# Kernel tuning notes

Hardware: AMD Instinct MI355X
Metric: run time of the kernel (lower is better)

Reference implementation:

```python
import jax, jax.numpy as jnp
import numpy as np

B, N, E, ENT, D, H, L = 64, 2048, 32768, 100000, 256, 256, 512


def setup_inputs() -> dict:
    key = jax.random.key(0)
    ks = jax.random.split(key, 12)
    return {
        "neighbors": jax.random.randint(ks[0], (B, N), 0, ENT),
        "adj_row": jax.random.randint(ks[1], (B, E), 0, N),
        "adj_col": jax.random.randint(ks[2], (B, E), 0, N),
        "adj_val": jax.random.uniform(ks[3], (B, E), dtype=jnp.float32),
        "emb_table": jax.random.normal(ks[4], (ENT, D), dtype=jnp.float32),
        "W1": jax.random.normal(ks[5], (D, H), dtype=jnp.float32) * (1.0 / np.sqrt(H)),
        "b1": jax.random.normal(ks[6], (H,), dtype=jnp.float32) * 0.01,
        "W2": jax.random.normal(ks[7], (H, H), dtype=jnp.float32) * (1.0 / np.sqrt(H)),
        "b2": jax.random.normal(ks[8], (H,), dtype=jnp.float32) * 0.01,
        "fc1_w": jax.random.normal(ks[9], (H, H), dtype=jnp.float32) * (1.0 / np.sqrt(H)),
        "fc1_b": jax.random.normal(ks[10], (H,), dtype=jnp.float32) * 0.01,
        "cur_len": L,
    }


def _gcn_layer(x, W, b, adj_row, adj_col, adj_val):
    # x: [B,N,din] -> support: [B,N,dout]
    support = jnp.einsum("bnd,dh->bnh", x, W)
    # sparse adj @ support: gather columns, scale by edge value, scatter-add to rows
    gathered = jnp.take_along_axis(support, adj_col[:, :, None], axis=1)  # [B,E,h]
    weighted = gathered * adj_val[:, :, None]
    agg = jax.vmap(lambda r, g: jax.ops.segment_sum(g, r, num_segments=N))(adj_row, weighted)
    return agg + b


def reference(neighbors, adj_row, adj_col, adj_val, emb_table, W1, b1, W2, b2, fc1_w, fc1_b, cur_len):
    x = emb_table[neighbors]                                   # [B,N,D] embedding gather
    x = _gcn_layer(x, W1, b1, adj_row, adj_col, adj_val)       # GCN layer 1
    x = _gcn_layer(x, W2, b2, adj_row, adj_col, adj_val)       # GCN layer 2
    seq = x[:, :cur_len, :]                                    # keep cur_node prefix, padded to common L
    pooled = jnp.mean(seq, axis=1, keepdims=True)              # self.seq == 'mean'
    return jax.nn.relu(jnp.einsum("blh,ho->blo", pooled, fc1_w) + fc1_b)  # [B,1,H]
```

## Files before the change

### kernel.cpp

```cpp
#include <hip/hip_runtime.h>

#define B 64
#define N 2048
#define E 32768
#define D 256
#define H 256
#define GCH 16
#define SEG 8
#define EPB (E / SEG)

__global__ __launch_bounds__(512) void edge_w_kernel(
    const int* __restrict__ adj_row, const int* __restrict__ adj_col,
    const float* __restrict__ adj_val, const int* __restrict__ cur_len,
    float* __restrict__ w_part, float* __restrict__ sw_part)
{
    __shared__ float wloc[N];
    __shared__ float sred[8];
    const int b = blockIdx.x, seg = blockIdx.y, tid = threadIdx.x;
    const int L = *cur_len;

    ((float4*)wloc)[tid] = make_float4(0.f, 0.f, 0.f, 0.f);
    __syncthreads();

    const int base = b * E + seg * EPB;
    float svp = 0.f;
    #pragma unroll
    for (int k = 0; k < EPB / 512; ++k) {
        const int e = base + tid + k * 512;
        const int r = adj_row[e];
        if (r < L) {
            const float v = adj_val[e];
            atomicAdd(&wloc[adj_col[e]], v);
            svp += v;
        }
    }
    __syncthreads();

    float4* dst = (float4*)(w_part + ((size_t)b * SEG + seg) * N);
    dst[tid] = ((const float4*)wloc)[tid];

    for (int off = 32; off; off >>= 1) svp += __shfl_down(svp, off, 64);
    if ((tid & 63) == 0) sred[tid >> 6] = svp;
    __syncthreads();
    if (tid == 0) {
        float s = 0.f;
        #pragma unroll
        for (int i = 0; i < 8; ++i) s += sred[i];
        sw_part[b * SEG + seg] = s;
    }
}

__global__ __launch_bounds__(512) void edge_z_kernel(
    const int* __restrict__ adj_row, const int* __restrict__ adj_col,
    const float* __restrict__ adj_val, const float* __restrict__ w_part,
    float* __restrict__ z_part)
{
    __shared__ float wfull[N];
    __shared__ float zloc[N];
    const int b = blockIdx.x, seg = blockIdx.y, tid = threadIdx.x;

    const float4* wp4 = (const float4*)(w_part + (size_t)b * SEG * N);
    float4 s = make_float4(0.f, 0.f, 0.f, 0.f);
    #pragma unroll
    for (int sg = 0; sg < SEG; ++sg) {
        const float4 v = wp4[sg * (N / 4) + tid];
        s.x += v.x; s.y += v.y; s.z += v.z; s.w += v.w;
    }
    ((float4*)wfull)[tid] = s;
    ((float4*)zloc)[tid]  = make_float4(0.f, 0.f, 0.f, 0.f);
    __syncthreads();

    const int base = b * E + seg * EPB;
    #pragma unroll
    for (int k = 0; k < EPB / 512; ++k) {
        const int e = base + tid + k * 512;
        const float wv = wfull[adj_row[e]];
        if (wv != 0.f) atomicAdd(&zloc[adj_col[e]], wv * adj_val[e]);
    }
    __syncthreads();

    float4* dst = (float4*)(z_part + ((size_t)b * SEG + seg) * N);
    dst[tid] = ((const float4*)zloc)[tid];
}

__global__ __launch_bounds__(256) void gather_kernel(
    const int* __restrict__ neighbors, const float* __restrict__ emb,
    const float* __restrict__ z_part, float* __restrict__ u_part)
{
    const int b = blockIdx.x, grp = blockIdx.y, tid = threadIdx.x;
    const int lane = tid & 63, rg = tid >> 6;
    const int n0 = grp * 128;

    __shared__ float zh[2][128];
    __shared__ int   ns[128];
    {
        const int j = tid & 127, half = tid >> 7;
        float s = 0.f;
        #pragma unroll
        for (int sg = 0; sg < SEG / 2; ++sg)
            s += z_part[((size_t)b * SEG + half * (SEG / 2) + sg) * N + n0 + j];
        zh[half][j] = s;
        if (half == 0) ns[j] = neighbors[(size_t)b * N + n0 + j];
    }
    __syncthreads();

    const float4* __restrict__ emb4 = (const float4*)emb;
    float4 a0 = make_float4(0.f,0.f,0.f,0.f), a1 = a0, a2 = a0, a3 = a0;

    #pragma unroll 8
    for (int i = 0; i < 32; ++i) {
        const int j = i * 4 + rg;
        const float zv = zh[0][j] + zh[1][j];
        const size_t idx = (size_t)ns[j];
        const float4 v = emb4[idx * (D / 4) + lane];
        if ((i & 3) == 0)      { a0.x += zv*v.x; a0.y += zv*v.y; a0.z += zv*v.z; a0.w += zv*v.w; }
        else if ((i & 3) == 1) { a1.x += zv*v.x; a1.y += zv*v.y; a1.z += zv*v.z; a1.w += zv*v.w; }
        else if ((i & 3) == 2) { a2.x += zv*v.x; a2.y += zv*v.y; a2.z += zv*v.z; a2.w += zv*v.w; }
        else                   { a3.x += zv*v.x; a3.y += zv*v.y; a3.z += zv*v.z; a3.w += zv*v.w; }
    }
    float4 acc = make_float4(a0.x+a1.x+a2.x+a3.x, a0.y+a1.y+a2.y+a3.y,
                             a0.z+a1.z+a2.z+a3.z, a0.w+a1.w+a2.w+a3.w);

    __shared__ float4 red[256];
    red[tid] = acc;
    __syncthreads();
    if (tid < 64) {
        float4 a = red[tid], bb = red[tid + 64], c = red[tid + 128], d = red[tid + 192];
        float4 s = make_float4(a.x + bb.x + c.x + d.x, a.y + bb.y + c.y + d.y,
                               a.z + bb.z + c.z + d.z, a.w + bb.w + c.w + d.w);
        ((float4*)u_part)[((size_t)b * GCH + grp) * (D / 4) + tid] = s;
    }
}

__global__ __launch_bounds__(1024) void head_kernel(
    const float* __restrict__ u_part, const float* __restrict__ sw_part,
    const float* __restrict__ W1, const float* __restrict__ b1,
    const float* __restrict__ W2, const float* __restrict__ b2,
    const float* __restrict__ fc1_w, const float* __restrict__ fc1_b,
    const int* __restrict__ cur_len, float* __restrict__ out)
{
    const int b = blockIdx.x;
    const int t = threadIdx.x & 255;
    const int s = threadIdx.x >> 8;
    __shared__ float red[4][256];
    __shared__ float su[D];
    __shared__ float sy[H];
    __shared__ float sp[H];

    float part = 0.f;
    #pragma unroll
    for (int c = 0; c < GCH / 4; ++c)
        part += u_part[((size_t)b * GCH + s * (GCH / 4) + c) * D + t];
    red[s][t] = part;
    __syncthreads();
    if (s == 0) su[t] = red[0][t] + red[1][t] + red[2][t] + red[3][t];
    __syncthreads();

    part = 0.f;
    #pragma unroll 8
    for (int k = 0; k < 64; ++k) {
        const int d = s * 64 + k;
        part += su[d] * W1[d * H + t];
    }
    red[s][t] = part;
    __syncthreads();
    if (s == 0) {
        float sw = 0.f;
        #pragma unroll
        for (int i = 0; i < SEG; ++i) sw += sw_part[b * SEG + i];
        sy[t] = red[0][t] + red[1][t] + red[2][t] + red[3][t] + sw * b1[t];
    }
    __syncthreads();

    const float invL = 1.f / (float)(*cur_len);
    part = 0.f;
    #pragma unroll 8
    for (int k = 0; k < 64; ++k) {
        const int d = s * 64 + k;
        part += sy[d] * W2[d * H + t];
    }
    red[s][t] = part;
    __syncthreads();
    if (s == 0)
        sp[t] = (red[0][t] + red[1][t] + red[2][t] + red[3][t]) * invL + b2[t];
    __syncthreads();

    part = 0.f;
    #pragma unroll 8
    for (int k = 0; k < 64; ++k) {
        const int d = s * 64 + k;
        part += sp[d] * fc1_w[d * H + t];
    }
    red[s][t] = part;
    __syncthreads();
    if (s == 0) {
        const float v = red[0][t] + red[1][t] + red[2][t] + red[3][t] + fc1_b[t];
        out[(size_t)b * H + t] = fmaxf(v, 0.f);
    }
}

extern "C" void kernel_launch(void* const* d_in, const int* in_sizes, int n_in,
                              void* d_out, int out_size, void* d_ws, size_t ws_size,
                              hipStream_t stream) {
    const int*   neighbors = (const int*)  d_in[0];
    const int*   adj_row   = (const int*)  d_in[1];
    const int*   adj_col   = (const int*)  d_in[2];
    const float* adj_val   = (const float*)d_in[3];
    const float* emb_table = (const float*)d_in[4];
    const float* W1        = (const float*)d_in[5];
    const float* b1        = (const float*)d_in[6];
    const float* W2        = (const float*)d_in[7];
    const float* b2        = (const float*)d_in[8];
    const float* fc1_w     = (const float*)d_in[9];
    const float* fc1_b     = (const float*)d_in[10];
    const int*   cur_len   = (const int*)  d_in[11];
    float*       out       = (float*)d_out;

    float* wp_ws = (float*)d_ws;
    float* zp_ws = wp_ws + (size_t)B * SEG * N;
    float* sw_ws = zp_ws + (size_t)B * SEG * N;
    float* u_ws  = sw_ws + (size_t)B * SEG;

    edge_w_kernel<<<dim3(B, SEG), 512, 0, stream>>>(adj_row, adj_col, adj_val,
                                                    cur_len, wp_ws, sw_ws);
    edge_z_kernel<<<dim3(B, SEG), 512, 0, stream>>>(adj_row, adj_col, adj_val,
                                                    wp_ws, zp_ws);
    gather_kernel<<<dim3(B, GCH), 256, 0, stream>>>(neighbors, emb_table, zp_ws, u_ws);
    head_kernel<<<B, 1024, 0, stream>>>(u_ws, sw_ws, W1, b1, W2, b2,
                                        fc1_w, fc1_b, cur_len, out);
}
```

Before: 225.5 us.

## Fuse head MLP into gather kernel via last-block atomic counter

Removes the separate head kernel launch. Each gather block bumps a per-batch atomic counter, and the last block of each batch reduces the partial sums and runs the three small matvecs with 256 threads. The counter is reset in edge_w_kernel. This saves one launch and its gap, but the tail matvecs now run on 256 threads per batch instead of 1024, which lengthens the serial tail.

Result: slower. 386.8 us (+71.6%).

```diff
diff --git a/kernel.cpp b/kernel.cpp
--- a/kernel.cpp
+++ b/kernel.cpp
@@ -12,13 +12,15 @@
 __global__ __launch_bounds__(512) void edge_w_kernel(
     const int* __restrict__ adj_row, const int* __restrict__ adj_col,
     const float* __restrict__ adj_val, const int* __restrict__ cur_len,
-    float* __restrict__ w_part, float* __restrict__ sw_part)
+    float* __restrict__ w_part, float* __restrict__ sw_part,
+    int* __restrict__ cnt)
 {
     __shared__ float wloc[N];
     __shared__ float sred[8];
     const int b = blockIdx.x, seg = blockIdx.y, tid = threadIdx.x;
     const int L = *cur_len;
 
+    if (seg == 0 && tid == 0) cnt[b] = 0;
     ((float4*)wloc)[tid] = make_float4(0.f, 0.f, 0.f, 0.f);
     __syncthreads();
 
@@ -83,9 +85,14 @@
     dst[tid] = ((const float4*)zloc)[tid];
 }
 
-__global__ __launch_bounds__(256) void gather_kernel(
+__global__ __launch_bounds__(256) void gather_head_kernel(
     const int* __restrict__ neighbors, const float* __restrict__ emb,
-    const float* __restrict__ z_part, float* __restrict__ u_part)
+    const float* __restrict__ z_part, float* __restrict__ u_part,
+    int* __restrict__ cnt, const float* __restrict__ sw_part,
+    const float* __restrict__ W1, const float* __restrict__ b1,
+    const float* __restrict__ W2, const float* __restrict__ b2,
+    const float* __restrict__ fc1_w, const float* __restrict__ fc1_b,
+    const int* __restrict__ cur_len, float* __restrict__ out)
 {
     const int b = blockIdx.x, grp = blockIdx.y, tid = threadIdx.x;
     const int lane = tid & 63, rg = tid >> 6;
@@ -130,73 +137,48 @@
                                a.z + bb.z + c.z + d.z, a.w + bb.w + c.w + d.w);
         ((float4*)u_part)[((size_t)b * GCH + grp) * (D / 4) + tid] = s;
     }
-}
-
-__global__ __launch_bounds__(1024) void head_kernel(
-    const float* __restrict__ u_part, const float* __restrict__ sw_part,
-    const float* __restrict__ W1, const float* __restrict__ b1,
-    const float* __restrict__ W2, const float* __restrict__ b2,
-    const float* __restrict__ fc1_w, const float* __restrict__ fc1_b,
-    const int* __restrict__ cur_len, float* __restrict__ out)
-{
-    const int b = blockIdx.x;
-    const int t = threadIdx.x & 255;
-    const int s = threadIdx.x >> 8;
-    __shared__ float red[4][256];
+    __syncthreads();
+
+    __shared__ int is_last;
+    __threadfence();
+    if (tid == 0) is_last = (atomicAdd(&cnt[b], 1) == GCH - 1) ? 1 : 0;
+    __syncthreads();
+    if (!is_last) return;
+    __threadfence();
+
     __shared__ float su[D];
     __shared__ float sy[H];
     __shared__ float sp[H];
-
-    float part = 0.f;
-    #pragma unroll
-    for (int c = 0; c < GCH / 4; ++c)
-        part += u_part[((size_t)b * GCH + s * (GCH / 4) + c) * D + t];
-    red[s][t] = part;
-    __syncthreads();
-    if (s == 0) su[t] = red[0][t] + red[1][t] + red[2][t] + red[3][t];
-    __syncthreads();
-
-    part = 0.f;
-    #pragma unroll 8
-    for (int k = 0; k < 64; ++k) {
-        const int d = s * 64 + k;
-        part += su[d] * W1[d * H + t];
-    }
-    red[s][t] = part;
-    __syncthreads();
-    if (s == 0) {
-        float sw = 0.f;
-        #pragma unroll
-        for (int i = 0; i < SEG; ++i) sw += sw_part[b * SEG + i];
-        sy[t] = red[0][t] + red[1][t] + red[2][t] + red[3][t] + sw * b1[t];
-    }
+    const int t = tid;
+
+    float uacc = 0.f;
+    #pragma unroll
+    for (int g = 0; g < GCH; ++g)
+        uacc += u_part[((size_t)b * GCH + g) * D + t];
+    su[t] = uacc;
+    __syncthreads();
+
+    float sw = 0.f;
+    #pragma unroll
+    for (int i = 0; i < SEG; ++i) sw += sw_part[b * SEG + i];
+
+    float v1 = sw * b1[t];
+    #pragma unroll 8
+    for (int d = 0; d < D; ++d) v1 += su[d] * W1[d * H + t];
+    sy[t] = v1;
     __syncthreads();
 
     const float invL = 1.f / (float)(*cur_len);
-    part = 0.f;
-    #pragma unroll 8
-    for (int k = 0; k < 64; ++k) {
-        const int d = s * 64 + k;
-        part += sy[d] * W2[d * H + t];
-    }
-    red[s][t] = part;
-    __syncthreads();
-    if (s == 0)
-        sp[t] = (red[0][t] + red[1][t] + red[2][t] + red[3][t]) * invL + b2[t];
-    __syncthreads();
-
-    part = 0.f;
-    #pragma unroll 8
-    for (int k = 0; k < 64; ++k) {
-        const int d = s * 64 + k;
-        part += sp[d] * fc1_w[d * H + t];
-    }
-    red[s][t] = part;
-    __syncthreads();
-    if (s == 0) {
-        const float v = red[0][t] + red[1][t] + red[2][t] + red[3][t] + fc1_b[t];
-        out[(size_t)b * H + t] = fmaxf(v, 0.f);
-    }
+    float v2 = 0.f;
+    #pragma unroll 8
+    for (int k = 0; k < H; ++k) v2 += sy[k] * W2[k * H + t];
+    sp[t] = v2 * invL + b2[t];
+    __syncthreads();
+
+    float v3 = fc1_b[t];
+    #pragma unroll 8
+    for (int k = 0; k < H; ++k) v3 += sp[k] * fc1_w[k * H + t];
+    out[(size_t)b * H + t] = fmaxf(v3, 0.f);
 }
 
 extern "C" void kernel_launch(void* const* d_in, const int* in_sizes, int n_in,
@@ -219,13 +201,14 @@
     float* wp_ws = (float*)d_ws;
     float* zp_ws = wp_ws + (size_t)B * SEG * N;
     float* sw_ws = zp_ws + (size_t)B * SEG * N;
-    float* u_ws  = sw_ws + (size_t)B * SEG;
+    int*   cnt   = (int*)(sw_ws + (size_t)B * SEG);
+    float* u_ws  = (float*)(cnt + B) + 60;
 
     edge_w_kernel<<<dim3(B, SEG), 512, 0, stream>>>(adj_row, adj_col, adj_val,
-                                                    cur_len, wp_ws, sw_ws);
+                                                    cur_len, wp_ws, sw_ws, cnt);
     edge_z_kernel<<<dim3(B, SEG), 512, 0, stream>>>(adj_row, adj_col, adj_val,
                                                     wp_ws, zp_ws);
-    gather_kernel<<<dim3(B, GCH), 256, 0, stream>>>(neighbors, emb_table, zp_ws, u_ws);
-    head_kernel<<<B, 1024, 0, stream>>>(u_ws, sw_ws, W1, b1, W2, b2,
-                                        fc1_w, fc1_b, cur_len, out);
-}
+    gather_head_kernel<<<dim3(B, GCH), 256, 0, stream>>>(
+        neighbors, emb_table, zp_ws, u_ws, cnt, sw_ws,
+        W1, b1, W2, b2, fc1_w, fc1_b, cur_len, out);
+}
```
